# Kernel optimization log

Hardware: AMD Instinct MI355X
Metric: run time of the kernel (lower is better)

Reference implementation:

```python
import jax, jax.numpy as jnp
import numpy as np

NEG_INF = -1e30
NEG_SLOPE = 0.2


def setup_inputs() -> dict:
    key = jax.random.key(0)
    k1, k2, k3, k4, k5 = jax.random.split(key, 5)
    B, N, D, H = 2, 2048, 512, 8
    k = D // H
    return {
        "x": jax.random.normal(k1, (B, N, D), dtype=jnp.float32),
        "A": jax.random.randint(k2, (B, N, N), 0, 2, dtype=jnp.int32),
        "W_proj": jax.random.normal(k3, (D, D), dtype=jnp.float32) * (1.0 / np.sqrt(D)),
        "W_att": jax.random.normal(k4, (H, 2 * k), dtype=jnp.float32) * (1.0 / np.sqrt(2 * k)),
        "b_att": jax.random.normal(k5, (H,), dtype=jnp.float32) * 0.01,
    }


def reference(x, A, W_proj, W_att, b_att):
    # x: [B, N, D_in]; A: [B, N, N]; W_proj: [D_in, D_out]; W_att: [H, 2k]; b_att: [H]
    B, N, _ = x.shape
    H, two_k = W_att.shape
    k = two_k // 2
    xp = jnp.einsum('bnd,do->bno', x, W_proj)            # [B, N, H*k]
    xh = xp.reshape(B, N, H, k).transpose(0, 2, 1, 3)    # [B, H, N, k]
    # Additive attention: score(i,j) = leaky_relu(w[:k]@x_i + w[k:]@x_j + b).
    # Decompose instead of materializing the O(N^2 * 2k) concat tensor.
    a_src = jnp.einsum('bhnk,hk->bhn', xh, W_att[:, :k])  # contribution of node i
    a_dst = jnp.einsum('bhnk,hk->bhn', xh, W_att[:, k:])  # contribution of node j
    scores = a_src[:, :, :, None] + a_dst[:, :, None, :] + b_att[None, :, None, None]
    scores = jax.nn.leaky_relu(scores, negative_slope=NEG_SLOPE)  # [B, H, N, N]
    mask = (A > 0)[:, None, :, :]
    scores = jnp.where(mask, scores, NEG_INF)
    att = jax.nn.softmax(scores, axis=-1)
    out = jax.nn.relu(jnp.einsum('bhij,bhjk->bhik', att, xh))  # [B, H, N, k]
    return out.transpose(0, 2, 1, 3).reshape(B, N, H * k)
```

## Files before the change

### kernel.cpp

```cpp
#include <hip/hip_runtime.h>
#include <cstdint>
#include <cstddef>

#define NEG_SLOPE 0.2f
#define LOG2E 1.4426950408889634f

#define BB 2
#define NN 2048
#define DD 512
#define HH 8
#define KK 64

typedef _Float16 half8 __attribute__((ext_vector_type(8)));
typedef _Float16 half4 __attribute__((ext_vector_type(4)));
typedef _Float16 half2v __attribute__((ext_vector_type(2)));
typedef float floatx4 __attribute__((ext_vector_type(4)));

#define X16T_OFF  ((size_t)0)
#define WT_OFF    ((size_t)4194304)
#define XHT_OFF   ((size_t)4718592)
#define ASRC_OFF  ((size_t)8912896)
#define AF_OFF    ((size_t)9043968)
#define ADMAX_OFF ((size_t)9175040)
#define MW_OFF    ((size_t)9183232)

#if __has_builtin(__builtin_amdgcn_global_load_lds)
#define GLL(gsrc, lbase, lane) \
    __builtin_amdgcn_global_load_lds((const __attribute__((address_space(1))) void*)(gsrc), \
                                     (__attribute__((address_space(3))) void*)(lbase), 16, 0, 0)
#else
#define GLL(gsrc, lbase, lane) \
    (*(uint4*)((char*)(lbase) + (size_t)(lane) * 16) = *(const uint4*)(gsrc))
#endif

__global__ __launch_bounds__(256) void k_pm(const int* __restrict__ A,
                                            const float* __restrict__ x,
                                            const float* __restrict__ Wp,
                                            unsigned long long* __restrict__ mwT,
                                            _Float16* __restrict__ x16t,
                                            _Float16* __restrict__ WT) {
    __shared__ float tile[64][65];
    __shared__ unsigned long long mwt[32][4];
    const int tid = threadIdx.x;
    const int bi = blockIdx.x;
    if (bi < 1024) {
        const int w = tid >> 6, lane = tid & 63;
        const int b = bi >> 9, n0 = (bi & 511) * 4;
        const int* Arow = A + ((size_t)b * NN + n0 + w) * NN + lane;
        int v[32];
#pragma unroll
        for (int c = 0; c < 32; ++c) v[c] = Arow[c * 64];
#pragma unroll
        for (int c = 0; c < 32; ++c) {
            unsigned long long m = __ballot(v[c] != 0);
            if (lane == 0) mwt[c][w] = m;
        }
        __syncthreads();
        if (tid < 128) {
            const int c = tid >> 2, rl = tid & 3;
            mwT[((size_t)b * 32 + c) * NN + n0 + rl] = mwt[c][rl];
        }
    } else if (bi < 1280) {
        const int xb = bi - 1024;
        const int r = tid & 15, cg = tid >> 4;
        const float* srow = x + (size_t)(xb * 16 + r) * DD;
        _Float16* obase = x16t + ((size_t)xb * 64) * 128 + r * 8;
#pragma unroll
        for (int q = 0; q < 4; ++q) {
            const int chunk = q * 16 + cg;
            float4 v0 = *(const float4*)(srow + chunk * 8);
            float4 v1 = *(const float4*)(srow + chunk * 8 + 4);
            half8 hv;
            hv[0] = (_Float16)v0.x; hv[1] = (_Float16)v0.y;
            hv[2] = (_Float16)v0.z; hv[3] = (_Float16)v0.w;
            hv[4] = (_Float16)v1.x; hv[5] = (_Float16)v1.y;
            hv[6] = (_Float16)v1.z; hv[7] = (_Float16)v1.w;
            *(half8*)(obase + (size_t)chunk * 128) = hv;
        }
    } else {
        const int wb = bi - 1280;
        const int d0 = (wb >> 3) * 64, o0 = (wb & 7) * 64;
        const int r = tid >> 2, cq = tid & 3;
#pragma unroll
        for (int qq = 0; qq < 4; ++qq) {
            float4 v = *(const float4*)&Wp[(size_t)(d0 + r) * DD + o0 + cq * 16 + qq * 4];
            tile[r][cq * 16 + qq * 4 + 0] = v.x;
            tile[r][cq * 16 + qq * 4 + 1] = v.y;
            tile[r][cq * 16 + qq * 4 + 2] = v.z;
            tile[r][cq * 16 + qq * 4 + 3] = v.w;
        }
        __syncthreads();
#pragma unroll
        for (int qq = 0; qq < 2; ++qq) {
            half8 hv;
#pragma unroll
            for (int e = 0; e < 8; ++e) hv[e] = (_Float16)tile[cq * 16 + qq * 8 + e][r];
            *(half8*)&WT[(size_t)(o0 + r) * DD + d0 + cq * 16 + qq * 8] = hv;
        }
    }
}

__global__ __launch_bounds__(256) void k_proj(const _Float16* __restrict__ x16t,
                                              const _Float16* __restrict__ WT,
                                              const float* __restrict__ Watt,
                                              _Float16* __restrict__ xhT2,
                                              float* __restrict__ asrc,
                                              unsigned* __restrict__ aFg,
                                              float* __restrict__ admax) {
    __shared__ __align__(16) _Float16 bt[64 * 512];
    const int tid = threadIdx.x;
    const int bi = blockIdx.x;
    const int mtile = bi >> 3, h = bi & 7;
    const int m0 = mtile * 64;
    {
        const int cir = tid & 63, wv4 = tid >> 6;
        const char* gsrc = (const char*)(WT + (size_t)h * 64 * DD);
        char* lbase = (char*)bt;
#pragma unroll
        for (int q = 0; q < 16; ++q) {
            const int row = q * 4 + wv4;
            *(uint4*)(lbase + row * 1024 + ((cir ^ (row & 7)) * 16)) =
                *(const uint4*)(gsrc + (size_t)row * 1024 + cir * 16);
        }
    }
    __syncthreads();
    const int w = tid >> 6, l = tid & 63, li = l & 15, p = l >> 4;
    const char* bbase = (const char*)bt;
    const _Float16* abase = x16t + ((size_t)(mtile * 4 + w)) * 64 * 128 + li * 8;
    floatx4 acc[4] = {};
    for (int k0 = 0; k0 < DD; k0 += 32) {
        const int ch = (k0 >> 3) + p;
        half8 a = *(const half8*)(abase + (size_t)ch * 128);
#pragma unroll
        for (int ct = 0; ct < 4; ++ct) {
            const int row = ct * 16 + li;
            half8 bfr = *(const half8*)(bbase + row * 1024 + ((ch ^ (li & 7)) * 16));
            acc[ct] = __builtin_amdgcn_mfma_f32_16x16x32_f16(a, bfr, acc[ct], 0, 0, 0);
        }
    }
    const int b = m0 >> 11, n0m = m0 & (NN - 1);
    const int c = n0m >> 6;
    const int bh = b * HH + h;
    {
        char* tb2 = (char*)xhT2 + ((size_t)(bh * 32 + c)) * 8192;
        const int colchunk = w * 2 + (p >> 1);
        const int sub = (p & 1) * 8;
#pragma unroll
        for (int ct = 0; ct < 4; ++ct) {
            const int kk = ct * 16 + li;
            half4 hv;
#pragma unroll
            for (int r = 0; r < 4; ++r) hv[r] = (_Float16)acc[ct][r];
            *(half4*)(tb2 + kk * 128 + ((colchunk ^ (kk & 7)) << 4) + sub) = hv;
        }
    }
    float w1[4], w2[4];
#pragma unroll
    for (int ct = 0; ct < 4; ++ct) {
        w1[ct] = Watt[h * 128 + ct * 16 + li];
        w2[ct] = Watt[h * 128 + 64 + ct * 16 + li];
    }
    float mx = -1e30f;
#pragma unroll
    for (int r = 0; r < 4; ++r) {
        float s1 = 0.f, s2 = 0.f;
#pragma unroll
        for (int ct = 0; ct < 4; ++ct) { s1 += acc[ct][r] * w1[ct]; s2 += acc[ct][r] * w2[ct]; }
#pragma unroll
        for (int d = 1; d < 16; d <<= 1) { s1 += __shfl_xor(s1, d, 64); s2 += __shfl_xor(s2, d, 64); }
        mx = fmaxf(mx, s2);
        if (li == 0) {
            const int n = n0m + w * 16 + p * 4 + r;
            asrc[bh * NN + n] = s1;
            const float bj = s2 * LOG2E;
            union { half2v h; unsigned u; } cv;
            cv.h[0] = (_Float16)exp2f(bj);
            cv.h[1] = (_Float16)exp2f(NEG_SLOPE * bj);
            aFg[bh * NN + n] = cv.u;
        }
    }
    mx = fmaxf(mx, __shfl_xor(mx, 16, 64));
    mx = fmaxf(mx, __shfl_xor(mx, 32, 64));
    if (l == 0) admax[bh * 128 + (mtile & 31) * 4 + w] = mx;
}

__global__ __launch_bounds__(256) void k_attn(const _Float16* __restrict__ xhT2,
                                              const float* __restrict__ asrc,
                                              const unsigned* __restrict__ aFg,
                                              const float* __restrict__ admax,
                                              const unsigned long long* __restrict__ mwT,
                                              const float* __restrict__ batt,
                                              float* __restrict__ out) {
    __shared__ __align__(16) _Float16 vt[2][2][4096];
    __shared__ __align__(16) unsigned aFl[2][2][64];
    __shared__ unsigned long long mwl[2][2][64];
    __shared__ float accd_s[2][32];
    __shared__ float amx_s;

    const int tid = threadIdx.x;
    const int w = tid >> 6, l = tid & 63, li = l & 15, p = l >> 4;
    const int g = w & 1, wr = w >> 1;
    const int bid = blockIdx.x;
    const int bh = bid >> 5, it = bid & 31;
    const int b = bh >> 3, h = bh & (HH - 1);
    const int i0 = it * 64;

    const _Float16* vbase = xhT2 + (size_t)bh * 32 * 4096;

    {
#pragma unroll
        for (int q = 0; q < 4; ++q) {
            const int chunk = (wr * 4 + q) * 64 + l;
            GLL(vbase + (size_t)g * 4096 + chunk * 8, &vt[g][0][(wr * 4 + q) * 512], l);
        }
        if (tid < 128) aFl[tid >> 6][0][tid & 63] =
            aFg[bh * NN + (tid >> 6) * 64 + (tid & 63)];
        if (tid < 128) mwl[tid >> 6][0][tid & 63] =
            mwT[((size_t)b * 32 + (tid >> 6)) * NN + i0 + (tid & 63)];
    }
    if (w == 0) {
        float mx = fmaxf(admax[bh * 128 + l], admax[bh * 128 + 64 + l]);
#pragma unroll
        for (int d = 1; d < 64; d <<= 1) mx = fmaxf(mx, __shfl_xor(mx, d, 64));
        if (l == 0) amx_s = mx;
    }
    __syncthreads();

    const float amL = amx_s * LOG2E;
    const float bbv = batt[h];
    const int ia = i0 + wr * 32 + li;
    const float aia = (asrc[bh * NN + ia] + bbv) * LOG2E;
    const float aib = (asrc[bh * NN + ia + 16] + bbv) * LOG2E;
    const float tba = aia + amL, tbb = aib + amL;
    const float Mia = fmaxf(tba, NEG_SLOPE * tba);
    const float Mib = fmaxf(tbb, NEG_SLOPE * tbb);
    half2v eh2a, eh2b;
    eh2a[0] = (_Float16)exp2f(aia - Mia); eh2a[1] = (_Float16)exp2f(NEG_SLOPE * aia - Mia);
    eh2b[0] = (_Float16)exp2f(aib - Mib); eh2b[1] = (_Float16)exp2f(NEG_SLOPE * aib - Mib);
    floatx4 acc0[4] = {}, acc1[4] = {};
    floatx4 accd0 = {}, accd1 = {};
    half8 ones;
#pragma unroll
    for (int e = 0; e < 8; ++e) ones[e] = (_Float16)1.0f;

    unsigned raF = 0; unsigned long long rmw = 0;
    for (int ci = 0; ci < 16; ++ci) {
        const int buf = ci & 1;
        char* vtg = (char*)&vt[g][buf][0];
        if (ci < 15) {
            const int cn = 2 * (ci + 1) + g;
#pragma unroll
            for (int q = 0; q < 4; ++q) {
                const int chunk = (wr * 4 + q) * 64 + l;
                GLL(vbase + (size_t)cn * 4096 + chunk * 8, &vt[g][buf ^ 1][(wr * 4 + q) * 512], l);
            }
            if (tid < 128) raF = aFg[bh * NN + (2 * (ci + 1) + (tid >> 6)) * 64 + (tid & 63)];
            if (tid < 128) rmw = mwT[((size_t)b * 32 + 2 * (ci + 1) + (tid >> 6)) * NN + i0 + (tid & 63)];
        }
        const unsigned long long mw0 = mwl[g][buf][wr * 32 + li];
        const unsigned long long mw1 = mwl[g][buf][wr * 32 + 16 + li];
#pragma unroll
        for (int js = 0; js < 2; ++js) {
            const int shbase = js * 32 + p * 8;
            uint4 F0 = *(const uint4*)&aFl[g][buf][shbase];
            uint4 F1 = *(const uint4*)&aFl[g][buf][shbase + 4];
            const unsigned m80 = (unsigned)(mw0 >> shbase) & 0xFFu;
            const unsigned m81 = (unsigned)(mw1 >> shbase) & 0xFFu;
            unsigned fb[8] = {F0.x, F0.y, F0.z, F0.w, F1.x, F1.y, F1.z, F1.w};
            half8 af0, af1;
#pragma unroll
            for (int e = 0; e < 8; ++e) {
                union { unsigned u; half2v h; } cv; cv.u = fb[e];
                half2v em0 = eh2a * cv.h;
                half2v em1 = eh2b * cv.h;
                _Float16 w0 = em0[0] > em0[1] ? em0[0] : em0[1];
                _Float16 w1v = em1[0] > em1[1] ? em1[0] : em1[1];
                af0[e] = ((m80 >> e) & 1u) ? w0 : (_Float16)0.f;
                af1[e] = ((m81 >> e) & 1u) ? w1v : (_Float16)0.f;
            }
            accd0 = __builtin_amdgcn_mfma_f32_16x16x32_f16(af0, ones, accd0, 0, 0, 0);
            accd1 = __builtin_amdgcn_mfma_f32_16x16x32_f16(af1, ones, accd1, 0, 0, 0);
#pragma unroll
            for (int ct = 0; ct < 4; ++ct) {
                const half8 bf = *(const half8*)(vtg + (ct * 16 + li) * 128 +
                                                 (((js * 4 + p) ^ (li & 7)) << 4));
                acc0[ct] = __builtin_amdgcn_mfma_f32_16x16x32_f16(af0, bf, acc0[ct], 0, 0, 0);
                acc1[ct] = __builtin_amdgcn_mfma_f32_16x16x32_f16(af1, bf, acc1[ct], 0, 0, 0);
            }
        }
        if (ci < 15) {
            if (tid < 128) aFl[tid >> 6][buf ^ 1][tid & 63] = raF;
            if (tid < 128) mwl[tid >> 6][buf ^ 1][tid & 63] = rmw;
        }
        __syncthreads();
    }

    float* accs = (float*)&vt[0][0][0];
    if (g == 1) {
#pragma unroll
        for (int ct = 0; ct < 4; ++ct)
#pragma unroll
            for (int r = 0; r < 4; ++r) {
                accs[(wr * 32 + p * 4 + r) * 64 + ct * 16 + li] = acc0[ct][r];
                accs[(wr * 32 + 16 + p * 4 + r) * 64 + ct * 16 + li] = acc1[ct][r];
            }
        if (li == 0) {
#pragma unroll
            for (int r = 0; r < 4; ++r) {
                accd_s[wr][p * 4 + r] = accd0[r];
                accd_s[wr][16 + p * 4 + r] = accd1[r];
            }
        }
    }
    __syncthreads();
    if (g == 0) {
#pragma unroll
        for (int f = 0; f < 2; ++f) {
#pragma unroll
            for (int r = 0; r < 4; ++r) {
                const floatx4* accf = f ? acc1 : acc0;
                const float da = (f ? accd1[r] : accd0[r]) + accd_s[wr][f * 16 + p * 4 + r];
                const float inv = 1.f / fmaxf(da, 1e-30f);
                const int irow = i0 + wr * 32 + f * 16 + p * 4 + r;
                float* orow = out + ((size_t)b * NN + irow) * DD + h * KK;
#pragma unroll
                for (int ct = 0; ct < 4; ++ct) {
                    const float v = (accf[ct][r] +
                                     accs[(wr * 32 + f * 16 + p * 4 + r) * 64 + ct * 16 + li]) * inv;
                    orow[ct * 16 + li] = fmaxf(v, 0.f);
                }
            }
        }
    }
}

extern "C" void kernel_launch(void* const* d_in, const int* in_sizes, int n_in,
                              void* d_out, int out_size, void* d_ws, size_t ws_size,
                              hipStream_t stream) {
    const float* x    = (const float*)d_in[0];
    const int*   A    = (const int*)d_in[1];
    const float* Wp   = (const float*)d_in[2];
    const float* Watt = (const float*)d_in[3];
    const float* batt = (const float*)d_in[4];
    float* out = (float*)d_out;

    char* ws = (char*)d_ws;
    _Float16* x16t = (_Float16*)(ws + X16T_OFF);
    _Float16* WT   = (_Float16*)(ws + WT_OFF);
    _Float16* xhT2 = (_Float16*)(ws + XHT_OFF);
    float* asrc  = (float*)(ws + ASRC_OFF);
    unsigned* aFg = (unsigned*)(ws + AF_OFF);
    float* admax = (float*)(ws + ADMAX_OFF);
    unsigned long long* mwT = (unsigned long long*)(ws + MW_OFF);

    k_pm<<<dim3(1344), 256, 0, stream>>>(A, x, Wp, mwT, x16t, WT);
    k_proj<<<dim3(512), 256, 0, stream>>>(x16t, WT, Watt, xhT2, asrc, aFg, admax);
    k_attn<<<dim3(BB * HH * 32), 256, 0, stream>>>(xhT2, asrc, aFg, admax, mwT, batt, out);
}
```

Baseline: 54.02 us.

## Split attention key loop across four wave groups with 512-thread blocks

The attention kernel doubles its block to 512 threads and splits the key dimension four ways instead of two, so each wave group runs 8 chunk iterations instead of 16. The partial accumulators are then merged through shared memory in a two-stage tree reduction. This raises per-block parallelism and shortens the serial loop, at the cost of twice the LDS for V tiles, extra reduction passes and barriers, and fewer co-resident blocks per CU.

```diff
diff --git a/kernel.cpp b/kernel.cpp
--- a/kernel.cpp
+++ b/kernel.cpp
@@ -184,22 +184,22 @@
     if (l == 0) admax[bh * 128 + (mtile & 31) * 4 + w] = mx;
 }
 
-__global__ __launch_bounds__(256) void k_attn(const _Float16* __restrict__ xhT2,
+__global__ __launch_bounds__(512) void k_attn(const _Float16* __restrict__ xhT2,
                                               const float* __restrict__ asrc,
                                               const unsigned* __restrict__ aFg,
                                               const float* __restrict__ admax,
                                               const unsigned long long* __restrict__ mwT,
                                               const float* __restrict__ batt,
                                               float* __restrict__ out) {
-    __shared__ __align__(16) _Float16 vt[2][2][4096];
-    __shared__ __align__(16) unsigned aFl[2][2][64];
-    __shared__ unsigned long long mwl[2][2][64];
-    __shared__ float accd_s[2][32];
+    __shared__ __align__(16) _Float16 vt[4][2][4096];
+    __shared__ __align__(16) unsigned aFl[4][2][64];
+    __shared__ unsigned long long mwl[4][2][64];
+    __shared__ float accd_sh[2][64];
     __shared__ float amx_s;
 
     const int tid = threadIdx.x;
     const int w = tid >> 6, l = tid & 63, li = l & 15, p = l >> 4;
-    const int g = w & 1, wr = w >> 1;
+    const int g = w & 3, wr = w >> 2;
     const int bid = blockIdx.x;
     const int bh = bid >> 5, it = bid & 31;
     const int b = bh >> 3, h = bh & (HH - 1);
@@ -213,9 +213,9 @@
             const int chunk = (wr * 4 + q) * 64 + l;
             GLL(vbase + (size_t)g * 4096 + chunk * 8, &vt[g][0][(wr * 4 + q) * 512], l);
         }
-        if (tid < 128) aFl[tid >> 6][0][tid & 63] =
+        if (tid < 256) aFl[tid >> 6][0][tid & 63] =
             aFg[bh * NN + (tid >> 6) * 64 + (tid & 63)];
-        if (tid < 128) mwl[tid >> 6][0][tid & 63] =
+        if (tid < 256) mwl[tid >> 6][0][tid & 63] =
             mwT[((size_t)b * 32 + (tid >> 6)) * NN + i0 + (tid & 63)];
     }
     if (w == 0) {
@@ -244,18 +244,18 @@
     for (int e = 0; e < 8; ++e) ones[e] = (_Float16)1.0f;
 
     unsigned raF = 0; unsigned long long rmw = 0;
-    for (int ci = 0; ci < 16; ++ci) {
+    for (int ci = 0; ci < 8; ++ci) {
         const int buf = ci & 1;
         char* vtg = (char*)&vt[g][buf][0];
-        if (ci < 15) {
-            const int cn = 2 * (ci + 1) + g;
+        if (ci < 7) {
+            const int cn = 4 * (ci + 1) + g;
 #pragma unroll
             for (int q = 0; q < 4; ++q) {
                 const int chunk = (wr * 4 + q) * 64 + l;
                 GLL(vbase + (size_t)cn * 4096 + chunk * 8, &vt[g][buf ^ 1][(wr * 4 + q) * 512], l);
             }
-            if (tid < 128) raF = aFg[bh * NN + (2 * (ci + 1) + (tid >> 6)) * 64 + (tid & 63)];
-            if (tid < 128) rmw = mwT[((size_t)b * 32 + 2 * (ci + 1) + (tid >> 6)) * NN + i0 + (tid & 63)];
+            if (tid < 256) raF = aFg[bh * NN + (4 * (ci + 1) + (tid >> 6)) * 64 + (tid & 63)];
+            if (tid < 256) rmw = mwT[((size_t)b * 32 + 4 * (ci + 1) + (tid >> 6)) * NN + i0 + (tid & 63)];
         }
         const unsigned long long mw0 = mwl[g][buf][wr * 32 + li];
         const unsigned long long mw1 = mwl[g][buf][wr * 32 + 16 + li];
@@ -288,27 +288,61 @@
                 acc1[ct] = __builtin_amdgcn_mfma_f32_16x16x32_f16(af1, bf, acc1[ct], 0, 0, 0);
             }
         }
-        if (ci < 15) {
-            if (tid < 128) aFl[tid >> 6][buf ^ 1][tid & 63] = raF;
-            if (tid < 128) mwl[tid >> 6][buf ^ 1][tid & 63] = rmw;
+        if (ci < 7) {
+            if (tid < 256) aFl[tid >> 6][buf ^ 1][tid & 63] = raF;
+            if (tid < 256) mwl[tid >> 6][buf ^ 1][tid & 63] = rmw;
         }
         __syncthreads();
     }
 
     float* accs = (float*)&vt[0][0][0];
+    if (g >= 2) {
+        const int slot = g - 2;
+#pragma unroll
+        for (int ct = 0; ct < 4; ++ct)
+#pragma unroll
+            for (int r = 0; r < 4; ++r) {
+                accs[slot * 4096 + (wr * 32 + p * 4 + r) * 64 + ct * 16 + li] = acc0[ct][r];
+                accs[slot * 4096 + (wr * 32 + 16 + p * 4 + r) * 64 + ct * 16 + li] = acc1[ct][r];
+            }
+        if (li == 0) {
+#pragma unroll
+            for (int r = 0; r < 4; ++r) {
+                accd_sh[slot][wr * 32 + p * 4 + r] = accd0[r];
+                accd_sh[slot][wr * 32 + 16 + p * 4 + r] = accd1[r];
+            }
+        }
+    }
+    __syncthreads();
+    if (g < 2) {
+        const int slot = g;
+#pragma unroll
+        for (int ct = 0; ct < 4; ++ct)
+#pragma unroll
+            for (int r = 0; r < 4; ++r) {
+                acc0[ct][r] += accs[slot * 4096 + (wr * 32 + p * 4 + r) * 64 + ct * 16 + li];
+                acc1[ct][r] += accs[slot * 4096 + (wr * 32 + 16 + p * 4 + r) * 64 + ct * 16 + li];
+            }
+#pragma unroll
+        for (int r = 0; r < 4; ++r) {
+            accd0[r] += accd_sh[slot][wr * 32 + p * 4 + r];
+            accd1[r] += accd_sh[slot][wr * 32 + 16 + p * 4 + r];
+        }
+    }
+    __syncthreads();
     if (g == 1) {
 #pragma unroll
         for (int ct = 0; ct < 4; ++ct)
 #pragma unroll
             for (int r = 0; r < 4; ++r) {
-                accs[(wr * 32 + p * 4 + r) * 64 + ct * 16 + li] = acc0[ct][r];
-                accs[(wr * 32 + 16 + p * 4 + r) * 64 + ct * 16 + li] = acc1[ct][r];
+                accs[4096 + (wr * 32 + p * 4 + r) * 64 + ct * 16 + li] = acc0[ct][r];
+                accs[4096 + (wr * 32 + 16 + p * 4 + r) * 64 + ct * 16 + li] = acc1[ct][r];
             }
         if (li == 0) {
 #pragma unroll
             for (int r = 0; r < 4; ++r) {
-                accd_s[wr][p * 4 + r] = accd0[r];
-                accd_s[wr][16 + p * 4 + r] = accd1[r];
+                accd_sh[1][wr * 32 + p * 4 + r] = accd0[r];
+                accd_sh[1][wr * 32 + 16 + p * 4 + r] = accd1[r];
             }
         }
     }
@@ -319,14 +353,14 @@
 #pragma unroll
             for (int r = 0; r < 4; ++r) {
                 const floatx4* accf = f ? acc1 : acc0;
-                const float da = (f ? accd1[r] : accd0[r]) + accd_s[wr][f * 16 + p * 4 + r];
+                const int rb = wr * 32 + f * 16 + p * 4 + r;
+                const float da = (f ? accd1[r] : accd0[r]) + accd_sh[1][rb];
                 const float inv = 1.f / fmaxf(da, 1e-30f);
-                const int irow = i0 + wr * 32 + f * 16 + p * 4 + r;
+                const int irow = i0 + rb;
                 float* orow = out + ((size_t)b * NN + irow) * DD + h * KK;
 #pragma unroll
                 for (int ct = 0; ct < 4; ++ct) {
-                    const float v = (accf[ct][r] +
-                                     accs[(wr * 32 + f * 16 + p * 4 + r) * 64 + ct * 16 + li]) * inv;
+                    const float v = (accf[ct][r] + accs[4096 + rb * 64 + ct * 16 + li]) * inv;
                     orow[ct * 16 + li] = fmaxf(v, 0.f);
                 }
             }
@@ -355,5 +389,5 @@
 
     k_pm<<<dim3(1344), 256, 0, stream>>>(A, x, Wp, mwT, x16t, WT);
     k_proj<<<dim3(512), 256, 0, stream>>>(x16t, WT, Watt, xhT2, asrc, aFg, admax);
-    k_attn<<<dim3(BB * HH * 32), 256, 0, stream>>>(xhT2, asrc, aFg, admax, mwT, batt, out);
+    k_attn<<<dim3(BB * HH * 32), 512, 0, stream>>>(xhT2, asrc, aFg, admax, mwT, batt, out);
 }
```

Measured after the change: 51.25 us. 5.1% less time.

## Split attention key range across four waves with per-wave buffers and no block syncs

Applied to the files above, without the earlier changes.

The attention kernel now gives each block 32 query rows instead of 64, doubling the block count. Each of the four waves takes a disjoint quarter of the 32-column key chunks and owns its own double-buffered LDS tile. Mask bits and exp factors come straight from global memory into registers instead of staging through shared memory. Per-iteration __syncthreads are replaced by explicit s_waitcnt on the wave's own loads, plus setprio around the MFMAs. The projection kernel's V layout is changed to 32-column chunks to match. In exchange, the epilogue must reduce partial sums from four waves through LDS, and each block does more per-row setup work.

```diff
diff --git a/kernel.cpp b/kernel.cpp
--- a/kernel.cpp
+++ b/kernel.cpp
@@ -139,19 +139,21 @@
         }
     }
     const int b = m0 >> 11, n0m = m0 & (NN - 1);
-    const int c = n0m >> 6;
     const int bh = b * HH + h;
     {
-        char* tb2 = (char*)xhT2 + ((size_t)(bh * 32 + c)) * 8192;
-        const int colchunk = w * 2 + (p >> 1);
-        const int sub = (p & 1) * 8;
+        const int jbase = w * 16 + p * 4;
+        const int c2 = (n0m + jbase) >> 5;
+        const int j_in = jbase & 31;
+        const int jc = j_in >> 3;
+        const int sub = (j_in & 7) * 2;
+        char* tb2 = (char*)xhT2 + ((size_t)(bh * 64 + c2)) * 4096;
 #pragma unroll
         for (int ct = 0; ct < 4; ++ct) {
             const int kk = ct * 16 + li;
             half4 hv;
 #pragma unroll
             for (int r = 0; r < 4; ++r) hv[r] = (_Float16)acc[ct][r];
-            *(half4*)(tb2 + kk * 128 + ((colchunk ^ (kk & 7)) << 4) + sub) = hv;
+            *(half4*)(tb2 + kk * 64 + ((jc ^ (kk & 3)) << 4) + sub) = hv;
         }
     }
     float w1[4], w2[4];
@@ -191,32 +193,33 @@
                                               const unsigned long long* __restrict__ mwT,
                                               const float* __restrict__ batt,
                                               float* __restrict__ out) {
-    __shared__ __align__(16) _Float16 vt[2][2][4096];
-    __shared__ __align__(16) unsigned aFl[2][2][64];
-    __shared__ unsigned long long mwl[2][2][64];
-    __shared__ float accd_s[2][32];
+    __shared__ __align__(16) _Float16 vt[4][2][2048];
+    __shared__ float accd_s[3][32];
     __shared__ float amx_s;
 
     const int tid = threadIdx.x;
     const int w = tid >> 6, l = tid & 63, li = l & 15, p = l >> 4;
-    const int g = w & 1, wr = w >> 1;
     const int bid = blockIdx.x;
-    const int bh = bid >> 5, it = bid & 31;
+    const int bh = bid >> 6, it = bid & 63;
     const int b = bh >> 3, h = bh & (HH - 1);
-    const int i0 = it * 64;
-
-    const _Float16* vbase = xhT2 + (size_t)bh * 32 * 4096;
-
+    const int i0 = it * 32;
+
+    const char* vbase = (const char*)(xhT2 + (size_t)bh * 64 * 2048);
+    const unsigned* fpb = aFg + bh * NN;
+    const unsigned* mw32 = (const unsigned*)mwT;
+    const size_t mrow0 = ((size_t)b * 32) * NN + i0 + li;
+
+    uint4 cf0, cf1; unsigned cm0, cm1;
     {
-#pragma unroll
-        for (int q = 0; q < 4; ++q) {
-            const int chunk = (wr * 4 + q) * 64 + l;
-            GLL(vbase + (size_t)g * 4096 + chunk * 8, &vt[g][0][(wr * 4 + q) * 512], l);
-        }
-        if (tid < 128) aFl[tid >> 6][0][tid & 63] =
-            aFg[bh * NN + (tid >> 6) * 64 + (tid & 63)];
-        if (tid < 128) mwl[tid >> 6][0][tid & 63] =
-            mwT[((size_t)b * 32 + (tid >> 6)) * NN + i0 + (tid & 63)];
+        const int c0 = w;
+        cf0 = *(const uint4*)&fpb[c0 * 32 + p * 8];
+        cf1 = *(const uint4*)&fpb[c0 * 32 + p * 8 + 4];
+        cm0 = mw32[(mrow0 + (size_t)(c0 >> 1) * NN) * 2 + (c0 & 1)];
+        cm1 = mw32[(mrow0 + 16 + (size_t)(c0 >> 1) * NN) * 2 + (c0 & 1)];
+        const char* srcb = vbase + (size_t)c0 * 4096;
+#pragma unroll
+        for (int q = 0; q < 4; ++q)
+            GLL(srcb + q * 1024 + l * 16, (char*)&vt[w][0][0] + q * 1024, l);
     }
     if (w == 0) {
         float mx = fmaxf(admax[bh * 128 + l], admax[bh * 128 + 64 + l]);
@@ -228,106 +231,107 @@
 
     const float amL = amx_s * LOG2E;
     const float bbv = batt[h];
-    const int ia = i0 + wr * 32 + li;
-    const float aia = (asrc[bh * NN + ia] + bbv) * LOG2E;
-    const float aib = (asrc[bh * NN + ia + 16] + bbv) * LOG2E;
-    const float tba = aia + amL, tbb = aib + amL;
-    const float Mia = fmaxf(tba, NEG_SLOPE * tba);
-    const float Mib = fmaxf(tbb, NEG_SLOPE * tbb);
-    half2v eh2a, eh2b;
-    eh2a[0] = (_Float16)exp2f(aia - Mia); eh2a[1] = (_Float16)exp2f(NEG_SLOPE * aia - Mia);
-    eh2b[0] = (_Float16)exp2f(aib - Mib); eh2b[1] = (_Float16)exp2f(NEG_SLOPE * aib - Mib);
+    const float ai0 = (asrc[bh * NN + i0 + li] + bbv) * LOG2E;
+    const float ai1 = (asrc[bh * NN + i0 + 16 + li] + bbv) * LOG2E;
+    const float tb0 = ai0 + amL, tb1 = ai1 + amL;
+    const float Mi0 = fmaxf(tb0, NEG_SLOPE * tb0);
+    const float Mi1 = fmaxf(tb1, NEG_SLOPE * tb1);
+    half2v eh0, eh1;
+    eh0[0] = (_Float16)exp2f(ai0 - Mi0); eh0[1] = (_Float16)exp2f(NEG_SLOPE * ai0 - Mi0);
+    eh1[0] = (_Float16)exp2f(ai1 - Mi1); eh1[1] = (_Float16)exp2f(NEG_SLOPE * ai1 - Mi1);
+
     floatx4 acc0[4] = {}, acc1[4] = {};
     floatx4 accd0 = {}, accd1 = {};
     half8 ones;
 #pragma unroll
     for (int e = 0; e < 8; ++e) ones[e] = (_Float16)1.0f;
 
-    unsigned raF = 0; unsigned long long rmw = 0;
-    for (int ci = 0; ci < 16; ++ci) {
-        const int buf = ci & 1;
-        char* vtg = (char*)&vt[g][buf][0];
-        if (ci < 15) {
-            const int cn = 2 * (ci + 1) + g;
-#pragma unroll
-            for (int q = 0; q < 4; ++q) {
-                const int chunk = (wr * 4 + q) * 64 + l;
-                GLL(vbase + (size_t)cn * 4096 + chunk * 8, &vt[g][buf ^ 1][(wr * 4 + q) * 512], l);
-            }
-            if (tid < 128) raF = aFg[bh * NN + (2 * (ci + 1) + (tid >> 6)) * 64 + (tid & 63)];
-            if (tid < 128) rmw = mwT[((size_t)b * 32 + 2 * (ci + 1) + (tid >> 6)) * NN + i0 + (tid & 63)];
-        }
-        const unsigned long long mw0 = mwl[g][buf][wr * 32 + li];
-        const unsigned long long mw1 = mwl[g][buf][wr * 32 + 16 + li];
-#pragma unroll
-        for (int js = 0; js < 2; ++js) {
-            const int shbase = js * 32 + p * 8;
-            uint4 F0 = *(const uint4*)&aFl[g][buf][shbase];
-            uint4 F1 = *(const uint4*)&aFl[g][buf][shbase + 4];
-            const unsigned m80 = (unsigned)(mw0 >> shbase) & 0xFFu;
-            const unsigned m81 = (unsigned)(mw1 >> shbase) & 0xFFu;
-            unsigned fb[8] = {F0.x, F0.y, F0.z, F0.w, F1.x, F1.y, F1.z, F1.w};
-            half8 af0, af1;
-#pragma unroll
-            for (int e = 0; e < 8; ++e) {
-                union { unsigned u; half2v h; } cv; cv.u = fb[e];
-                half2v em0 = eh2a * cv.h;
-                half2v em1 = eh2b * cv.h;
-                _Float16 w0 = em0[0] > em0[1] ? em0[0] : em0[1];
-                _Float16 w1v = em1[0] > em1[1] ? em1[0] : em1[1];
-                af0[e] = ((m80 >> e) & 1u) ? w0 : (_Float16)0.f;
-                af1[e] = ((m81 >> e) & 1u) ? w1v : (_Float16)0.f;
-            }
-            accd0 = __builtin_amdgcn_mfma_f32_16x16x32_f16(af0, ones, accd0, 0, 0, 0);
-            accd1 = __builtin_amdgcn_mfma_f32_16x16x32_f16(af1, ones, accd1, 0, 0, 0);
-#pragma unroll
-            for (int ct = 0; ct < 4; ++ct) {
-                const half8 bf = *(const half8*)(vtg + (ct * 16 + li) * 128 +
-                                                 (((js * 4 + p) ^ (li & 7)) << 4));
-                acc0[ct] = __builtin_amdgcn_mfma_f32_16x16x32_f16(af0, bf, acc0[ct], 0, 0, 0);
-                acc1[ct] = __builtin_amdgcn_mfma_f32_16x16x32_f16(af1, bf, acc1[ct], 0, 0, 0);
-            }
-        }
-        if (ci < 15) {
-            if (tid < 128) aFl[tid >> 6][buf ^ 1][tid & 63] = raF;
-            if (tid < 128) mwl[tid >> 6][buf ^ 1][tid & 63] = rmw;
-        }
-        __syncthreads();
-    }
-
+    for (int t = 0; t < 16; ++t) {
+        const int buf = t & 1;
+        uint4 nf0 = cf0, nf1 = cf1; unsigned nm0 = cm0, nm1 = cm1;
+        if (t < 15) {
+            const int cn = 4 * (t + 1) + w;
+            nf0 = *(const uint4*)&fpb[cn * 32 + p * 8];
+            nf1 = *(const uint4*)&fpb[cn * 32 + p * 8 + 4];
+            nm0 = mw32[(mrow0 + (size_t)(cn >> 1) * NN) * 2 + (cn & 1)];
+            nm1 = mw32[(mrow0 + 16 + (size_t)(cn >> 1) * NN) * 2 + (cn & 1)];
+            const char* srcb = vbase + (size_t)cn * 4096;
+#pragma unroll
+            for (int q = 0; q < 4; ++q)
+                GLL(srcb + q * 1024 + l * 16, (char*)&vt[w][buf ^ 1][0] + q * 1024, l);
+        }
+        __builtin_amdgcn_sched_barrier(0);
+        if (t < 15) __builtin_amdgcn_s_waitcnt(0x0F78);
+        else        __builtin_amdgcn_s_waitcnt(0x0F70);
+        __builtin_amdgcn_sched_barrier(0);
+
+        const char* vtg = (const char*)&vt[w][buf][0];
+        const unsigned m80 = (cm0 >> (p * 8)) & 0xFFu;
+        const unsigned m81 = (cm1 >> (p * 8)) & 0xFFu;
+        const unsigned fv[8] = {cf0.x, cf0.y, cf0.z, cf0.w, cf1.x, cf1.y, cf1.z, cf1.w};
+        half8 af0, af1;
+#pragma unroll
+        for (int e = 0; e < 8; ++e) {
+            union { unsigned u; half2v h; } cv; cv.u = fv[e];
+            half2v em0 = eh0 * cv.h;
+            half2v em1 = eh1 * cv.h;
+            _Float16 w0 = em0[0] > em0[1] ? em0[0] : em0[1];
+            _Float16 w1v = em1[0] > em1[1] ? em1[0] : em1[1];
+            af0[e] = ((m80 >> e) & 1u) ? w0 : (_Float16)0.f;
+            af1[e] = ((m81 >> e) & 1u) ? w1v : (_Float16)0.f;
+        }
+        __builtin_amdgcn_s_setprio(1);
+        accd0 = __builtin_amdgcn_mfma_f32_16x16x32_f16(af0, ones, accd0, 0, 0, 0);
+        accd1 = __builtin_amdgcn_mfma_f32_16x16x32_f16(af1, ones, accd1, 0, 0, 0);
+#pragma unroll
+        for (int ct = 0; ct < 4; ++ct) {
+            const int kk = ct * 16 + li;
+            const half8 bf = *(const half8*)(vtg + kk * 64 + ((p ^ (kk & 3)) << 4));
+            acc0[ct] = __builtin_amdgcn_mfma_f32_16x16x32_f16(af0, bf, acc0[ct], 0, 0, 0);
+            acc1[ct] = __builtin_amdgcn_mfma_f32_16x16x32_f16(af1, bf, acc1[ct], 0, 0, 0);
+        }
+        __builtin_amdgcn_s_setprio(0);
+        cf0 = nf0; cf1 = nf1; cm0 = nm0; cm1 = nm1;
+    }
+
+    __syncthreads();
     float* accs = (float*)&vt[0][0][0];
-    if (g == 1) {
+    if (w != 0) {
+        const int s = w - 1;
 #pragma unroll
         for (int ct = 0; ct < 4; ++ct)
 #pragma unroll
             for (int r = 0; r < 4; ++r) {
-                accs[(wr * 32 + p * 4 + r) * 64 + ct * 16 + li] = acc0[ct][r];
-                accs[(wr * 32 + 16 + p * 4 + r) * 64 + ct * 16 + li] = acc1[ct][r];
+                accs[s * 2048 + (p * 4 + r) * 64 + ct * 16 + li] = acc0[ct][r];
+                accs[s * 2048 + (16 + p * 4 + r) * 64 + ct * 16 + li] = acc1[ct][r];
             }
         if (li == 0) {
 #pragma unroll
             for (int r = 0; r < 4; ++r) {
-                accd_s[wr][p * 4 + r] = accd0[r];
-                accd_s[wr][16 + p * 4 + r] = accd1[r];
+                accd_s[s][p * 4 + r] = accd0[r];
+                accd_s[s][16 + p * 4 + r] = accd1[r];
             }
         }
     }
     __syncthreads();
-    if (g == 0) {
+    if (w == 0) {
 #pragma unroll
         for (int f = 0; f < 2; ++f) {
 #pragma unroll
             for (int r = 0; r < 4; ++r) {
+                const int row = f * 16 + p * 4 + r;
+                float d = (f ? accd1[r] : accd0[r]) +
+                          accd_s[0][row] + accd_s[1][row] + accd_s[2][row];
+                const float inv = 1.f / fmaxf(d, 1e-30f);
+                float* orow = out + ((size_t)b * NN + i0 + row) * DD + h * KK;
                 const floatx4* accf = f ? acc1 : acc0;
-                const float da = (f ? accd1[r] : accd0[r]) + accd_s[wr][f * 16 + p * 4 + r];
-                const float inv = 1.f / fmaxf(da, 1e-30f);
-                const int irow = i0 + wr * 32 + f * 16 + p * 4 + r;
-                float* orow = out + ((size_t)b * NN + irow) * DD + h * KK;
 #pragma unroll
                 for (int ct = 0; ct < 4; ++ct) {
-                    const float v = (accf[ct][r] +
-                                     accs[(wr * 32 + f * 16 + p * 4 + r) * 64 + ct * 16 + li]) * inv;
-                    orow[ct * 16 + li] = fmaxf(v, 0.f);
+                    const int col = ct * 16 + li;
+                    const float v = (accf[ct][r] + accs[0 * 2048 + row * 64 + col] +
+                                     accs[1 * 2048 + row * 64 + col] +
+                                     accs[2 * 2048 + row * 64 + col]) * inv;
+                    orow[col] = fmaxf(v, 0.f);
                 }
             }
         }
@@ -355,5 +359,5 @@
 
     k_pm<<<dim3(1344), 256, 0, stream>>>(A, x, Wp, mwT, x16t, WT);
     k_proj<<<dim3(512), 256, 0, stream>>>(x16t, WT, Watt, xhT2, asrc, aFg, admax);
-    k_attn<<<dim3(BB * HH * 32), 256, 0, stream>>>(xhT2, asrc, aFg, admax, mwT, batt, out);
+    k_attn<<<dim3(BB * HH * 64), 256, 0, stream>>>(xhT2, asrc, aFg, admax, mwT, batt, out);
 }
```

New measurement: 52.83 us. 1.02x faster.
